# Performance work log

Measured on AMD Instinct MI355X. Metric: run time of the kernel, lower is better.

## Reference

```python
import jax, jax.numpy as jnp
import numpy as np

B, T, D_MODEL, D_HIDDEN, MAX_SEQLEN = 4, 2048, 1024, 1024, 2048


def setup_inputs() -> dict:
    key = jax.random.key(0)
    ks = jax.random.split(key, 8)
    scale = 0.02  # keep exp() and linear outputs in a sane range
    return {
        "q": jax.random.normal(ks[0], (B, T, D_MODEL), dtype=jnp.float32),
        "k": jax.random.normal(ks[1], (B, T, D_MODEL), dtype=jnp.float32),
        "v": jax.random.normal(ks[2], (B, T, D_MODEL), dtype=jnp.float32),
        "Wq": jax.random.normal(ks[3], (D_HIDDEN, D_MODEL), dtype=jnp.float32) * scale,
        "Wk": jax.random.normal(ks[4], (D_HIDDEN, D_MODEL), dtype=jnp.float32) * scale,
        "Wv": jax.random.normal(ks[5], (D_HIDDEN, D_MODEL), dtype=jnp.float32) * scale,
        "Wo": jax.random.normal(ks[6], (D_MODEL, D_HIDDEN), dtype=jnp.float32) * scale,
        "W_bias": jax.random.normal(ks[7], (MAX_SEQLEN, MAX_SEQLEN), dtype=jnp.float32) * scale,
    }


def reference(q, k, v, Wq, Wk, Wv, Wo, W_bias):
    Ti = q.shape[1]
    Tj = k.shape[1]
    # Linear projections (torch Linear: x @ W.T), bias=False
    Q = jnp.einsum('btm,hm->bth', q, Wq)
    K = jnp.einsum('btm,hm->bth', k, Wk)
    V = jnp.einsum('btm,hm->bth', v, Wv)
    pos_bias = W_bias[:Ti, :Tj][None]              # (1, Ti, Tj)
    # Faithful to original: max over dim 0 (batch dim for K, singleton dim for pos_bias)
    max_key = jnp.max(K, axis=0, keepdims=True)    # (1, Tj, Dh)
    max_pos_bias = jnp.max(pos_bias, axis=0, keepdims=True)  # == pos_bias (dim 0 is size 1)
    exp_key = jnp.exp(K - max_key)                 # (B, Tj, Dh)
    exp_pos_bias = jnp.exp(pos_bias - max_pos_bias)  # all-ones, kept for faithfulness
    num = jnp.einsum('bij,bjd->bid', exp_pos_bias, exp_key * V)
    den = jnp.einsum('bij,bjd->bid', exp_pos_bias, exp_key)
    Yt = jax.nn.sigmoid(Q) * num / den             # (B, Ti, Dh)
    return jnp.einsum('bth,mh->btm', Yt, Wo)
```

## Files before the change

kernel.cpp:

```cpp
#include <hip/hip_runtime.h>
#include <hip/hip_bf16.h>

typedef __bf16 bf16;
typedef __bf16 bf16x8 __attribute__((ext_vector_type(8)));
typedef __bf16 bf16x4 __attribute__((ext_vector_type(4)));
typedef float f32x4 __attribute__((ext_vector_type(4)));

#define B_   4
#define T_   2048
#define DM_  1024
#define DH_  1024
#define MROWS 8192

struct CvtJob { const float* src; bf16* dst; int nf4; };
struct CvtArgs { CvtJob job[7]; };

__global__ __launch_bounds__(256) void cvt_kernel(CvtArgs args) {
  CvtJob jb = args.job[blockIdx.y];
  int base = blockIdx.x * 2048;
  if (base >= jb.nf4) return;
  int t2 = threadIdx.x * 2;
  const float4* s = (const float4*)jb.src;
  float4 a[4][2];
#pragma unroll
  for (int u = 0; u < 4; ++u) {
    a[u][0] = s[base + u * 512 + t2];
    a[u][1] = s[base + u * 512 + t2 + 1];
  }
#pragma unroll
  for (int u = 0; u < 4; ++u) {
    bf16x8 o;
    o[0] = (bf16)a[u][0].x; o[1] = (bf16)a[u][0].y;
    o[2] = (bf16)a[u][0].z; o[3] = (bf16)a[u][0].w;
    o[4] = (bf16)a[u][1].x; o[5] = (bf16)a[u][1].y;
    o[6] = (bf16)a[u][1].z; o[7] = (bf16)a[u][1].w;
    *(bf16x8*)(jb.dst + ((size_t)base + u * 512 + t2) * 4) = o;
  }
}

struct GemmJob { const bf16* A; const bf16* Bw; float* Cf; bf16* Cb; int mode; };
struct GemmArgs { GemmJob job[4]; int N; int K; };

__global__ __launch_bounds__(256) void gemm_bt(GemmArgs ga) {
  const GemmJob jb = ga.job[blockIdx.z];
  const int N = ga.N, K = ga.K;
  __shared__ bf16 As[128 * 64];
  __shared__ bf16 Bs[128 * 64];

  const int tid  = threadIdx.x;
  const int lane = tid & 63;
  const int wave = tid >> 6;
  const int wm   = (wave >> 1) * 64;
  const int wn   = (wave & 1) * 64;

  const int f   = blockIdx.y * 8 + blockIdx.x;
  const int xcd = f & 7;
  const int j   = f >> 3;
  const int bn  = j & 7;
  const int bm  = (j >> 3) * 8 + xcd;
  const int tileM = bm * 128;
  const int tileN = bn * 128;

  f32x4 acc[4][4] = {};

  const int sr = lane >> 3;
  const int sc = (lane & 7) ^ sr;

  for (int k0 = 0; k0 < K; k0 += 64) {
#pragma unroll
    for (int l = 0; l < 4; ++l) {
      int grp = wave * 4 + l;
      int row = grp * 8 + sr;
      const bf16* gaadr = jb.A + (size_t)(tileM + row) * K + k0 + sc * 8;
      __builtin_amdgcn_global_load_lds(
          (const __attribute__((address_space(1))) void*)gaadr,
          (__attribute__((address_space(3))) void*)&As[grp * 512], 16, 0, 0);
      const bf16* gbadr = jb.Bw + (size_t)(tileN + row) * K + k0 + sc * 8;
      __builtin_amdgcn_global_load_lds(
          (const __attribute__((address_space(1))) void*)gbadr,
          (__attribute__((address_space(3))) void*)&Bs[grp * 512], 16, 0, 0);
    }
    __syncthreads();

    const int quad = lane >> 4;
#pragma unroll
    for (int s = 0; s < 2; ++s) {
      bf16x8 af[4], bfr[4];
#pragma unroll
      for (int mt = 0; mt < 4; ++mt) {
        int row = wm + mt * 16 + (lane & 15);
        int chunk = (s * 4 + quad) ^ (row & 7);
        af[mt] = *(const bf16x8*)&As[row * 64 + chunk * 8];
      }
#pragma unroll
      for (int nt = 0; nt < 4; ++nt) {
        int row = wn + nt * 16 + (lane & 15);
        int chunk = (s * 4 + quad) ^ (row & 7);
        bfr[nt] = *(const bf16x8*)&Bs[row * 64 + chunk * 8];
      }
#pragma unroll
      for (int mt = 0; mt < 4; ++mt)
#pragma unroll
        for (int nt = 0; nt < 4; ++nt)
          acc[mt][nt] = __builtin_amdgcn_mfma_f32_16x16x32_bf16(
              af[mt], bfr[nt], acc[mt][nt], 0, 0, 0);
    }
    __syncthreads();
  }

  const int cn = lane & 15;
  const int cr = (lane >> 4) * 4;
  if (jb.mode == 0) {
#pragma unroll
    for (int mt = 0; mt < 4; ++mt)
#pragma unroll
      for (int nt = 0; nt < 4; ++nt)
#pragma unroll
        for (int r = 0; r < 4; ++r) {
          int row = tileM + wm + mt * 16 + cr + r;
          int col = tileN + wn + nt * 16 + cn;
          jb.Cf[(size_t)row * N + col] = acc[mt][nt][r];
        }
  } else if (jb.mode == 1) {
#pragma unroll
    for (int mt = 0; mt < 4; ++mt)
#pragma unroll
      for (int nt = 0; nt < 4; ++nt)
#pragma unroll
        for (int r = 0; r < 4; ++r) {
          int row = tileM + wm + mt * 16 + cr + r;
          int col = tileN + wn + nt * 16 + cn;
          jb.Cb[(size_t)row * N + col] =
              (bf16)(1.f / (1.f + __expf(-acc[mt][nt][r])));
        }
  } else {
#pragma unroll
    for (int mt = 0; mt < 4; ++mt)
#pragma unroll
      for (int nt = 0; nt < 4; ++nt)
#pragma unroll
        for (int r = 0; r < 4; ++r) {
          int row = tileM + wm + mt * 16 + cr + r;
          int col = tileN + wn + nt * 16 + cn;
          jb.Cb[(size_t)row * N + col] = (bf16)acc[mt][nt][r];
        }
  }
}

__global__ __launch_bounds__(256) void reduce_kv(
    const bf16* __restrict__ Kb, const bf16* __restrict__ Vb,
    float* __restrict__ part) {
  __shared__ float lds[64 * 128];
  const int t = threadIdx.x;
  const int half = t >> 7;
  const int dt = t & 127;
  const int d = dt * 8;
  const int j0 = blockIdx.x * 8 + half * 4;
  const size_t bs = (size_t)T_ * DH_;
  float n[4][8] = {}, e[4][8] = {};
  for (int jj = j0; jj < j0 + 4; ++jj) {
    size_t off = (size_t)jj * DH_ + d;
    bf16x8 kk[4], vv[4];
#pragma unroll
    for (int b = 0; b < 4; ++b) {
      kk[b] = *(const bf16x8*)(Kb + off + b * bs);
      vv[b] = *(const bf16x8*)(Vb + off + b * bs);
    }
#pragma unroll
    for (int c = 0; c < 8; ++c) {
      float k0 = (float)kk[0][c], k1 = (float)kk[1][c];
      float k2 = (float)kk[2][c], k3 = (float)kk[3][c];
      float m = fmaxf(fmaxf(k0, k1), fmaxf(k2, k3));
      float w0 = __expf(k0 - m), w1 = __expf(k1 - m);
      float w2 = __expf(k2 - m), w3 = __expf(k3 - m);
      e[0][c] += w0; e[1][c] += w1; e[2][c] += w2; e[3][c] += w3;
      n[0][c] += w0 * (float)vv[0][c];
      n[1][c] += w1 * (float)vv[1][c];
      n[2][c] += w2 * (float)vv[2][c];
      n[3][c] += w3 * (float)vv[3][c];
    }
  }
  if (half) {
#pragma unroll
    for (int b = 0; b < 4; ++b)
#pragma unroll
      for (int c = 0; c < 8; ++c) {
        lds[(b * 8 + c) * 128 + dt] = n[b][c];
        lds[(32 + b * 8 + c) * 128 + dt] = e[b][c];
      }
  }
  __syncthreads();
  if (!half) {
    float* po = part + (size_t)blockIdx.x * 8192;
#pragma unroll
    for (int b = 0; b < 4; ++b)
#pragma unroll
      for (int c = 0; c < 8; ++c) {
        po[b * 1024 + d + c] = n[b][c] + lds[(b * 8 + c) * 128 + dt];
        po[4096 + b * 1024 + d + c] = e[b][c] + lds[(32 + b * 8 + c) * 128 + dt];
      }
  }
}

__global__ __launch_bounds__(256) void finish_kv(
    const float* __restrict__ part, float* __restrict__ numden) {
  __shared__ float lds[128];
  const int t = threadIdx.x;
  const int half = t >> 7;
  const int sl = t & 127;
  const int slot = blockIdx.x * 128 + sl;
  float s = 0.f;
  for (int i = half * 128; i < half * 128 + 128; i += 8) {
#pragma unroll
    for (int u = 0; u < 8; ++u)
      s += part[(size_t)(i + u) * 8192 + slot];
  }
  if (half) lds[sl] = s;
  __syncthreads();
  if (!half) numden[slot] = s + lds[sl];
}

__global__ __launch_bounds__(256) void mul_ratio(
    bf16* __restrict__ Yb, const float* __restrict__ num,
    const float* __restrict__ den) {
  size_t i = ((size_t)blockIdx.x * 256 + threadIdx.x) * 8;
  int h = (int)(i & (DH_ - 1));
  int b = (int)(i >> 21);
  bf16x8 y = *(bf16x8*)(Yb + i);
  const float* nu = num + b * DH_ + h;
  const float* de = den + b * DH_ + h;
  float4 n0 = *(const float4*)nu;
  float4 n1 = *(const float4*)(nu + 4);
  float4 d0 = *(const float4*)de;
  float4 d1 = *(const float4*)(de + 4);
  bf16x8 o;
  o[0] = (bf16)((float)y[0] * n0.x / d0.x);
  o[1] = (bf16)((float)y[1] * n0.y / d0.y);
  o[2] = (bf16)((float)y[2] * n0.z / d0.z);
  o[3] = (bf16)((float)y[3] * n0.w / d0.w);
  o[4] = (bf16)((float)y[4] * n1.x / d1.x);
  o[5] = (bf16)((float)y[5] * n1.y / d1.y);
  o[6] = (bf16)((float)y[6] * n1.z / d1.z);
  o[7] = (bf16)((float)y[7] * n1.w / d1.w);
  *(bf16x8*)(Yb + i) = o;
}

extern "C" void kernel_launch(void* const* d_in, const int* in_sizes, int n_in,
                              void* d_out, int out_size, void* d_ws, size_t ws_size,
                              hipStream_t stream) {
  const float* q  = (const float*)d_in[0];
  const float* k  = (const float*)d_in[1];
  const float* v  = (const float*)d_in[2];
  const float* Wq = (const float*)d_in[3];
  const float* Wk = (const float*)d_in[4];
  const float* Wv = (const float*)d_in[5];
  const float* Wo = (const float*)d_in[6];
  float* out = (float*)d_out;

  char* ws = (char*)d_ws;
  size_t off = 0;
  auto alloc = [&](size_t bytes) {
    char* p = ws + off;
    off += (bytes + 255) & ~(size_t)255;
    return p;
  };
  const size_t actN = (size_t)MROWS * DM_;
  const size_t wN   = (size_t)DH_ * DM_;

  bf16* qb  = (bf16*)alloc(actN * 2);
  bf16* kb  = (bf16*)alloc(actN * 2);
  bf16* vb  = (bf16*)alloc(actN * 2);
  bf16* Wqb = (bf16*)alloc(wN * 2);
  bf16* Wkb = (bf16*)alloc(wN * 2);
  bf16* Wvb = (bf16*)alloc(wN * 2);
  bf16* Wob = (bf16*)alloc(wN * 2);
  bf16* Kb  = (bf16*)alloc(actN * 2);
  bf16* Vb  = (bf16*)alloc(actN * 2);
  bf16* Yb  = (bf16*)alloc(actN * 2);
  float* part = (float*)alloc((size_t)256 * 8192 * 4);
  float* numden = (float*)alloc(8192 * 4);
  float* num = numden;
  float* den = numden + 4096;

  CvtArgs ca;
  ca.job[0] = {q,  qb,  (int)(actN / 4)};
  ca.job[1] = {k,  kb,  (int)(actN / 4)};
  ca.job[2] = {v,  vb,  (int)(actN / 4)};
  ca.job[3] = {Wq, Wqb, (int)(wN / 4)};
  ca.job[4] = {Wk, Wkb, (int)(wN / 4)};
  ca.job[5] = {Wv, Wvb, (int)(wN / 4)};
  ca.job[6] = {Wo, Wob, (int)(wN / 4)};
  cvt_kernel<<<dim3(actN / 4 / 2048, 7), 256, 0, stream>>>(ca);

  GemmArgs g1;
  g1.N = DH_; g1.K = DM_;
  g1.job[0] = {kb, Wkb, nullptr, Kb, 2};
  g1.job[1] = {vb, Wvb, nullptr, Vb, 2};
  g1.job[2] = {qb, Wqb, nullptr, Yb, 1};
  g1.job[3] = {nullptr, nullptr, nullptr, nullptr, 0};
  gemm_bt<<<dim3(8, MROWS / 128, 3), 256, 0, stream>>>(g1);

  reduce_kv<<<dim3(256), 256, 0, stream>>>(Kb, Vb, part);
  finish_kv<<<dim3(64), 256, 0, stream>>>(part, numden);

  mul_ratio<<<dim3(actN / 8 / 256), 256, 0, stream>>>(Yb, num, den);

  GemmArgs g2;
  g2.N = DM_; g2.K = DH_;
  g2.job[0] = {Yb, Wob, out, nullptr, 0};
  g2.job[1] = g2.job[2] = g2.job[3] = {nullptr, nullptr, nullptr, nullptr, 0};
  gemm_bt<<<dim3(8, MROWS / 128, 1), 256, 0, stream>>>(g2);
}
```

Baseline: 279.4 us.

## Fold num/den ratio into per-batch scaled Wo and simplify GEMM address math

Instead of scaling the full 8192x1024 Y activation by num/den, the per-batch, per-hidden ratio is folded into a per-batch copy of Wo (4x1M elements). The final GEMM runs as four batch jobs, each using its own scaled weight. The GEMM load loop also precomputes byte offsets and advances pointers each k-step instead of recomputing full addresses. This trades an elementwise pass over 8M elements for one over 4M and slightly less L2 reuse of Wo, and it reuses the partials buffer as storage.

```diff
diff --git a/kernel.cpp b/kernel.cpp
--- a/kernel.cpp
+++ b/kernel.cpp
@@ -66,23 +66,31 @@
   const int sr = lane >> 3;
   const int sc = (lane & 7) ^ sr;
 
+  const char* pa = (const char*)(jb.A  + (size_t)tileM * K);
+  const char* pb = (const char*)(jb.Bw + (size_t)tileN * K);
+  unsigned int off[4];
+#pragma unroll
+  for (int l = 0; l < 4; ++l)
+    off[l] = (unsigned int)((((wave * 4 + l) * 8 + sr) * K + sc * 8) * 2);
+
+  const int quad = lane >> 4;
+
   for (int k0 = 0; k0 < K; k0 += 64) {
 #pragma unroll
     for (int l = 0; l < 4; ++l) {
-      int grp = wave * 4 + l;
-      int row = grp * 8 + sr;
-      const bf16* gaadr = jb.A + (size_t)(tileM + row) * K + k0 + sc * 8;
       __builtin_amdgcn_global_load_lds(
-          (const __attribute__((address_space(1))) void*)gaadr,
-          (__attribute__((address_space(3))) void*)&As[grp * 512], 16, 0, 0);
-      const bf16* gbadr = jb.Bw + (size_t)(tileN + row) * K + k0 + sc * 8;
+          (const __attribute__((address_space(1))) void*)(pa + off[l]),
+          (__attribute__((address_space(3))) void*)&As[(wave * 4 + l) * 512],
+          16, 0, 0);
       __builtin_amdgcn_global_load_lds(
-          (const __attribute__((address_space(1))) void*)gbadr,
-          (__attribute__((address_space(3))) void*)&Bs[grp * 512], 16, 0, 0);
+          (const __attribute__((address_space(1))) void*)(pb + off[l]),
+          (__attribute__((address_space(3))) void*)&Bs[(wave * 4 + l) * 512],
+          16, 0, 0);
     }
+    pa += 128;
+    pb += 128;
     __syncthreads();
 
-    const int quad = lane >> 4;
 #pragma unroll
     for (int s = 0; s < 2; ++s) {
       bf16x8 af[4], bfr[4];
@@ -220,29 +228,29 @@
   if (!half) numden[slot] = s + lds[sl];
 }
 
-__global__ __launch_bounds__(256) void mul_ratio(
-    bf16* __restrict__ Yb, const float* __restrict__ num,
-    const float* __restrict__ den) {
+__global__ __launch_bounds__(256) void scale_wo(
+    const bf16* __restrict__ Wo, const float* __restrict__ numden,
+    bf16* __restrict__ out4) {
+  const int b = blockIdx.y;
   size_t i = ((size_t)blockIdx.x * 256 + threadIdx.x) * 8;
   int h = (int)(i & (DH_ - 1));
-  int b = (int)(i >> 21);
-  bf16x8 y = *(bf16x8*)(Yb + i);
-  const float* nu = num + b * DH_ + h;
-  const float* de = den + b * DH_ + h;
+  bf16x8 w = *(const bf16x8*)(Wo + i);
+  const float* nu = numden + b * DH_ + h;
+  const float* de = numden + 4096 + b * DH_ + h;
   float4 n0 = *(const float4*)nu;
   float4 n1 = *(const float4*)(nu + 4);
   float4 d0 = *(const float4*)de;
   float4 d1 = *(const float4*)(de + 4);
   bf16x8 o;
-  o[0] = (bf16)((float)y[0] * n0.x / d0.x);
-  o[1] = (bf16)((float)y[1] * n0.y / d0.y);
-  o[2] = (bf16)((float)y[2] * n0.z / d0.z);
-  o[3] = (bf16)((float)y[3] * n0.w / d0.w);
-  o[4] = (bf16)((float)y[4] * n1.x / d1.x);
-  o[5] = (bf16)((float)y[5] * n1.y / d1.y);
-  o[6] = (bf16)((float)y[6] * n1.z / d1.z);
-  o[7] = (bf16)((float)y[7] * n1.w / d1.w);
-  *(bf16x8*)(Yb + i) = o;
+  o[0] = (bf16)((float)w[0] * n0.x / d0.x);
+  o[1] = (bf16)((float)w[1] * n0.y / d0.y);
+  o[2] = (bf16)((float)w[2] * n0.z / d0.z);
+  o[3] = (bf16)((float)w[3] * n0.w / d0.w);
+  o[4] = (bf16)((float)w[4] * n1.x / d1.x);
+  o[5] = (bf16)((float)w[5] * n1.y / d1.y);
+  o[6] = (bf16)((float)w[6] * n1.z / d1.z);
+  o[7] = (bf16)((float)w[7] * n1.w / d1.w);
+  *(bf16x8*)(out4 + (size_t)b * ((size_t)DM_ * DH_) + i) = o;
 }
 
 extern "C" void kernel_launch(void* const* d_in, const int* in_sizes, int n_in,
@@ -279,8 +287,7 @@
   bf16* Yb  = (bf16*)alloc(actN * 2);
   float* part = (float*)alloc((size_t)256 * 8192 * 4);
   float* numden = (float*)alloc(8192 * 4);
-  float* num = numden;
-  float* den = numden + 4096;
+  bf16* Wob4 = (bf16*)part;
 
   CvtArgs ca;
   ca.job[0] = {q,  qb,  (int)(actN / 4)};
@@ -303,11 +310,15 @@
   reduce_kv<<<dim3(256), 256, 0, stream>>>(Kb, Vb, part);
   finish_kv<<<dim3(64), 256, 0, stream>>>(part, numden);
 
-  mul_ratio<<<dim3(actN / 8 / 256), 256, 0, stream>>>(Yb, num, den);
+  scale_wo<<<dim3(512, 4), 256, 0, stream>>>(Wob, numden, Wob4);
 
   GemmArgs g2;
   g2.N = DM_; g2.K = DH_;
-  g2.job[0] = {Yb, Wob, out, nullptr, 0};
-  g2.job[1] = g2.job[2] = g2.job[3] = {nullptr, nullptr, nullptr, nullptr, 0};
-  gemm_bt<<<dim3(8, MROWS / 128, 1), 256, 0, stream>>>(g2);
-}
+  for (int b = 0; b < 4; ++b) {
+    g2.job[b] = {Yb + (size_t)b * ((size_t)T_ * DH_),
+                 Wob4 + (size_t)b * wN,
+                 out + (size_t)b * ((size_t)T_ * DM_),
+                 nullptr, 0};
+  }
+  gemm_bt<<<dim3(8, 16, 4), 256, 0, stream>>>(g2);
+}
```

Measured after the change: 278.9 us. No clear change (-0.2%).
